# Performance work log

Measured on AMD Instinct MI355X. Metric: run time of the kernel, lower is better.

Reference implementation:

```python
import jax, jax.numpy as jnp
import numpy as np

B, N, D_IN, D_OUT, H = 4, 2048, 1024, 1024, 16
HEAD_DIM = D_OUT // H


def setup_inputs() -> dict:
    key = jax.random.key(0)
    k1, k2, k3 = jax.random.split(key, 3)
    x = jax.random.normal(k1, (B, N, D_IN), dtype=jnp.float32)
    # torch Linear: y = x @ W.T + b; we store W already transposed as [in, out]
    w_attn = jax.random.normal(k2, (D_IN, 3 * D_OUT), dtype=jnp.float32) * (1.0 / np.sqrt(D_IN))
    w_proj = jax.random.normal(k3, (D_OUT, D_OUT), dtype=jnp.float32) * (1.0 / np.sqrt(D_OUT))
    b_proj = jnp.zeros((D_OUT,), dtype=jnp.float32)
    return {"x": x, "w_attn": w_attn, "w_proj": w_proj, "b_proj": b_proj}


def reference(x, w_attn, w_proj, b_proj):
    b, n, _ = x.shape
    qkv = x @ w_attn  # [b, n, 3*d_out]
    q, k, v = jnp.split(qkv, 3, axis=2)
    # [b, n, d_out] -> [b, h, n, head_dim]
    def to_heads(t):
        return t.reshape(b, n, H, HEAD_DIM).transpose(0, 2, 1, 3)
    q, k, v = to_heads(q), to_heads(k), to_heads(v)
    scale = 1.0 / np.sqrt(HEAD_DIM).astype(np.float32)
    att = jnp.einsum('bhqd,bhkd->bhqk', q, k) * scale  # [b, h, n, n]
    causal = jnp.tril(jnp.ones((n, n), dtype=bool))  # True = keep
    att = jnp.where(causal, att, -jnp.inf)
    att = jax.nn.softmax(att, axis=-1)
    # dropout p=0.0 -> identity
    out = jnp.einsum('bhqk,bhkd->bhqd', att, v)  # [b, h, n, head_dim]
    out = out.transpose(0, 2, 1, 3).reshape(b, n, D_OUT)
    return out @ w_proj + b_proj
```

## Files before the change

kernel.cpp:

```cpp
#include <hip/hip_runtime.h>
#include <hip/hip_bf16.h>
#include <stdint.h>

typedef short short8 __attribute__((ext_vector_type(8)));
typedef float f32x4 __attribute__((ext_vector_type(4)));

#define BQ 4
#define NSEQ 2048
#define DMODEL 1024
#define NHEAD 16
#define HDIM 64
#define MTOT 8192
#define QKV_LD 3072

#if __has_builtin(__builtin_amdgcn_exp2f)
#define EXP2(x) __builtin_amdgcn_exp2f(x)
#else
#define EXP2(x) exp2f(x)
#endif
#define C_SCL 0.18033688f
#define THR_RAW 16.635532f

__device__ __forceinline__ uint16_t f2bf(float f) {
  uint32_t u = __builtin_bit_cast(uint32_t, f);
  uint32_t r = (u + 0x7FFFu + ((u >> 16) & 1u)) >> 16;
  return (uint16_t)r;
}
__device__ __forceinline__ uint16_t f2bf_hw(float f) {
  __hip_bfloat16 h = __float2bfloat16(f);
  return __builtin_bit_cast(uint16_t, h);
}

__global__ void cast_f32_bf16_k(const float* __restrict__ in, uint16_t* __restrict__ out, int n) {
  int idx = (blockIdx.x * blockDim.x + threadIdx.x) * 4;
  int stride = gridDim.x * blockDim.x * 4;
  for (int i = idx; i < n; i += stride) {
    float4 v = *reinterpret_cast<const float4*>(in + i);
    ushort4 o;
    o.x = f2bf(v.x); o.y = f2bf(v.y); o.z = f2bf(v.z); o.w = f2bf(v.w);
    *reinterpret_cast<ushort4*>(out + i) = o;
  }
}

__global__ void transpose_cast_k(const float* __restrict__ in, uint16_t* __restrict__ out, int K, int N) {
  __shared__ float tile[32][33];
  int n0 = blockIdx.x * 32;
  int k0 = blockIdx.y * 32;
  int tx = threadIdx.x & 31;
  int ty = threadIdx.x >> 5;
#pragma unroll
  for (int r = 0; r < 4; ++r)
    tile[ty + r * 8][tx] = in[(size_t)(k0 + ty + r * 8) * N + n0 + tx];
  __syncthreads();
#pragma unroll
  for (int r = 0; r < 4; ++r)
    out[(size_t)(n0 + ty + r * 8) * K + k0 + tx] = f2bf(tile[tx][ty + r * 8]);
}

template <bool BF16_OUT>
__global__ void __launch_bounds__(256, 2)
gemm_bt_k(const uint16_t* __restrict__ A, const uint16_t* __restrict__ BT,
          void* __restrict__ Cout, const float* __restrict__ bias,
          int M, int N, int K) {
  __shared__ uint16_t As[128 * 32];
  __shared__ uint16_t Bs[128 * 32];
  const int tid = threadIdx.x;
  const int lane = tid & 63;
  const int wave = tid >> 6;
  const int wr = wave >> 1, wc = wave & 1;
  const int brow = blockIdx.y * 128;
  const int bcol = blockIdx.x * 128;
  const int l16 = lane & 15;
  const int lq = lane >> 4;

  f32x4 acc[4][4];
  const f32x4 fzero = {0.f, 0.f, 0.f, 0.f};
#pragma unroll
  for (int i = 0; i < 4; ++i)
#pragma unroll
    for (int j = 0; j < 4; ++j) acc[i][j] = fzero;

  const int ca = tid, cb = tid + 256;
  const size_t ga0 = (size_t)(brow + (ca >> 2)) * K + (ca & 3) * 8;
  const size_t ga1 = (size_t)(brow + (cb >> 2)) * K + (cb & 3) * 8;
  const size_t gb0 = (size_t)(bcol + (ca >> 2)) * K + (ca & 3) * 8;
  const size_t gb1 = (size_t)(bcol + (cb >> 2)) * K + (cb & 3) * 8;

  for (int kt = 0; kt < K; kt += 32) {
    __builtin_amdgcn_global_load_lds(
        (const __attribute__((address_space(1))) void*)(A + ga0 + kt),
        (__attribute__((address_space(3))) void*)&As[ca * 8], 16, 0, 0);
    __builtin_amdgcn_global_load_lds(
        (const __attribute__((address_space(1))) void*)(A + ga1 + kt),
        (__attribute__((address_space(3))) void*)&As[cb * 8], 16, 0, 0);
    __builtin_amdgcn_global_load_lds(
        (const __attribute__((address_space(1))) void*)(BT + gb0 + kt),
        (__attribute__((address_space(3))) void*)&Bs[ca * 8], 16, 0, 0);
    __builtin_amdgcn_global_load_lds(
        (const __attribute__((address_space(1))) void*)(BT + gb1 + kt),
        (__attribute__((address_space(3))) void*)&Bs[cb * 8], 16, 0, 0);
    __syncthreads();
    short8 af[4], bfr[4];
#pragma unroll
    for (int r = 0; r < 4; ++r) {
      af[r]  = *reinterpret_cast<const short8*>(&As[(wr * 64 + r * 16 + l16) * 32 + lq * 8]);
      bfr[r] = *reinterpret_cast<const short8*>(&Bs[(wc * 64 + r * 16 + l16) * 32 + lq * 8]);
    }
#pragma unroll
    for (int r = 0; r < 4; ++r)
#pragma unroll
      for (int c = 0; c < 4; ++c)
        acc[r][c] = __builtin_amdgcn_mfma_f32_16x16x32_bf16(af[r], bfr[c], acc[r][c], 0, 0, 0);
    __syncthreads();
  }

#pragma unroll
  for (int r = 0; r < 4; ++r) {
    const int row0 = brow + wr * 64 + r * 16 + lq * 4;
#pragma unroll
    for (int c = 0; c < 4; ++c) {
      const int col = bcol + wc * 64 + c * 16 + l16;
#pragma unroll
      for (int i = 0; i < 4; ++i) {
        if constexpr (BF16_OUT)
          reinterpret_cast<uint16_t*>(Cout)[(size_t)(row0 + i) * N + col] = f2bf(acc[r][c][i]);
        else
          reinterpret_cast<float*>(Cout)[(size_t)(row0 + i) * N + col] = acc[r][c][i] + bias[col];
      }
    }
  }
}

__global__ void __launch_bounds__(256, 3)
attn_fwd_k(const uint16_t* __restrict__ qkv, uint16_t* __restrict__ outb) {
  const int obid = blockIdx.x;
  const int bid = (obid & 7) * 128 + (obid >> 3);
  const int p = bid & 15;
  const int h = (bid >> 4) & 15;
  const int b = bid >> 8;
  const int qtA = p;
  const int qtB = 31 - p;
  const int tid = threadIdx.x;
  const int lane = tid & 63;
  const int w = tid >> 6;
  const int l16 = lane & 15;
  const int lq = lane >> 4;

  __shared__ uint16_t Ks[64 * 72];
  __shared__ uint16_t Vt[64 * 72];

  short8 qaA0, qaA1, qaB0, qaB1;
  {
    const size_t baseA = ((size_t)(b * NSEQ + qtA * 64 + w * 16 + l16)) * QKV_LD + h * 64 + lq * 8;
    const size_t baseB = ((size_t)(b * NSEQ + qtB * 64 + w * 16 + l16)) * QKV_LD + h * 64 + lq * 8;
    qaA0 = *reinterpret_cast<const short8*>(qkv + baseA);
    qaA1 = *reinterpret_cast<const short8*>(qkv + baseA + 32);
    qaB0 = *reinterpret_cast<const short8*>(qkv + baseB);
    qaB1 = *reinterpret_cast<const short8*>(qkv + baseB + 32);
  }

  float mA = -1e30f, lA = 0.f, mB = -1e30f, lB = 0.f;
  f32x4 accA[4], accB[4];
  const f32x4 fzero = {0.f, 0.f, 0.f, 0.f};
#pragma unroll
  for (int i = 0; i < 4; ++i) { accA[i] = fzero; accB[i] = fzero; }

  const int r0 = tid >> 3, d0 = (tid & 7) * 8;
  const int ka0 = r0 * 72 + d0;
  const int ka1 = (r0 + 32) * 72 + d0;
  const int lqt = (r0 >> 2) & 3;
  const int nc0 = r0 >> 4;
  const int m0 = d0 >> 3;
  const int jo = (nc0 & 1) * 4 + (r0 & 3);
  const int vcol0 = (((2 * lqt) ^ m0) * 8) + jo;
  const int vcol1 = (((2 * lqt + 1) ^ m0) * 8) + jo;

  const int ntiles = qtB + 1;
  short8 rk0, rk1, rv0, rv1;
  {
    const size_t g0 = ((size_t)(b * NSEQ + r0)) * QKV_LD + 1024 + h * 64 + d0;
    const size_t g1 = ((size_t)(b * NSEQ + r0 + 32)) * QKV_LD + 1024 + h * 64 + d0;
    rk0 = *reinterpret_cast<const short8*>(qkv + g0);
    rv0 = *reinterpret_cast<const short8*>(qkv + g0 + 1024);
    rk1 = *reinterpret_cast<const short8*>(qkv + g1);
    rv1 = *reinterpret_cast<const short8*>(qkv + g1 + 1024);
  }

#define SOFTMAX_PV(SV, M_I, L_I, ACC, DIAG)                                     \
  {                                                                             \
    float tmax_ = -3e38f;                                                       \
    if (DIAG) {                                                                 \
      _Pragma("unroll") for (int nc = 0; nc < 4; ++nc) {                        \
        _Pragma("unroll") for (int i = 0; i < 4; ++i) {                         \
          float v_ = SV[nc][i];                                                 \
          if ((nc * 16 + lq * 4 + i) > (w * 16 + l16)) v_ = -3e38f;             \
          SV[nc][i] = v_;                                                       \
          tmax_ = fmaxf(tmax_, v_);                                             \
        }                                                                       \
      }                                                                         \
    } else {                                                                    \
      _Pragma("unroll") for (int nc = 0; nc < 4; ++nc)                          \
        tmax_ = fmaxf(tmax_, fmaxf(fmaxf(SV[nc][0], SV[nc][1]),                 \
                                   fmaxf(SV[nc][2], SV[nc][3])));               \
    }                                                                           \
    tmax_ = fmaxf(tmax_, __shfl_xor(tmax_, 16, 64));                            \
    tmax_ = fmaxf(tmax_, __shfl_xor(tmax_, 32, 64));                            \
    if (!__all(tmax_ <= M_I + THR_RAW)) {                                       \
      const float mn_ = fmaxf(M_I, tmax_);                                      \
      const float alpha_ = EXP2((M_I - mn_) * C_SCL);                           \
      M_I = mn_;                                                                \
      L_I *= alpha_;                                                            \
      float ab_[4];                                                             \
      _Pragma("unroll") for (int i = 0; i < 4; ++i)                             \
        ab_[i] = __shfl(alpha_, lq * 4 + i, 64);                                \
      _Pragma("unroll") for (int d4 = 0; d4 < 4; ++d4)                          \
        _Pragma("unroll") for (int i = 0; i < 4; ++i)                           \
          ACC[d4][i] *= ab_[i];                                                 \
    }                                                                           \
    const float mc_ = M_I * C_SCL;                                              \
    float rsum_ = 0.f;                                                          \
    short8 pa0_, pa1_;                                                          \
    _Pragma("unroll") for (int nc = 0; nc < 4; ++nc) {                          \
      _Pragma("unroll") for (int i = 0; i < 4; ++i) {                           \
        float pv_ = EXP2(__builtin_fmaf(SV[nc][i], C_SCL, -mc_));               \
        rsum_ += pv_;                                                           \
        uint16_t ph_ = f2bf_hw(pv_);                                            \
        if (nc < 2) pa0_[nc * 4 + i] = (short)ph_;                              \
        else        pa1_[(nc - 2) * 4 + i] = (short)ph_;                        \
      }                                                                         \
    }                                                                           \
    rsum_ += __shfl_xor(rsum_, 16, 64);                                         \
    rsum_ += __shfl_xor(rsum_, 32, 64);                                         \
    L_I += rsum_;                                                               \
    _Pragma("unroll") for (int d4 = 0; d4 < 4; ++d4) {                          \
      const int drow_ = d4 * 16 + l16;                                          \
      const int xr_ = (drow_ >> 3) & 7;                                         \
      short8 vb0_ = *reinterpret_cast<const short8*>(&Vt[drow_ * 72 + (((2 * lq) ^ xr_) * 8)]); \
      short8 vb1_ = *reinterpret_cast<const short8*>(&Vt[drow_ * 72 + (((2 * lq + 1) ^ xr_) * 8)]); \
      ACC[d4] = __builtin_amdgcn_mfma_f32_16x16x32_bf16(pa0_, vb0_, ACC[d4], 0, 0, 0); \
      ACC[d4] = __builtin_amdgcn_mfma_f32_16x16x32_bf16(pa1_, vb1_, ACC[d4], 0, 0, 0); \
    }                                                                           \
  }

  for (int jt = 0; jt < ntiles; ++jt) {
    *reinterpret_cast<short8*>(&Ks[ka0]) = rk0;
    *reinterpret_cast<short8*>(&Ks[ka1]) = rk1;
#pragma unroll
    for (int j = 0; j < 8; ++j) Vt[(d0 + j) * 72 + vcol0] = (uint16_t)rv0[j];
#pragma unroll
    for (int j = 0; j < 8; ++j) Vt[(d0 + j) * 72 + vcol1] = (uint16_t)rv1[j];
    if (jt + 1 < ntiles) {
      const size_t g0 = ((size_t)(b * NSEQ + (jt + 1) * 64 + r0)) * QKV_LD + 1024 + h * 64 + d0;
      const size_t g1 = ((size_t)(b * NSEQ + (jt + 1) * 64 + r0 + 32)) * QKV_LD + 1024 + h * 64 + d0;
      rk0 = *reinterpret_cast<const short8*>(qkv + g0);
      rv0 = *reinterpret_cast<const short8*>(qkv + g0 + 1024);
      rk1 = *reinterpret_cast<const short8*>(qkv + g1);
      rv1 = *reinterpret_cast<const short8*>(qkv + g1 + 1024);
    }
    __syncthreads();

    {
      f32x4 sv[4];
#pragma unroll
      for (int nc = 0; nc < 4; ++nc) {
        short8 kb0 = *reinterpret_cast<const short8*>(&Ks[(nc * 16 + l16) * 72 + lq * 8]);
        short8 kb1 = *reinterpret_cast<const short8*>(&Ks[(nc * 16 + l16) * 72 + 32 + lq * 8]);
        f32x4 s = fzero;
        s = __builtin_amdgcn_mfma_f32_16x16x32_bf16(kb0, qaB0, s, 0, 0, 0);
        s = __builtin_amdgcn_mfma_f32_16x16x32_bf16(kb1, qaB1, s, 0, 0, 0);
        sv[nc] = s;
      }
      SOFTMAX_PV(sv, mB, lB, accB, jt == qtB);
    }

    if (jt <= qtA) {
      f32x4 sv[4];
#pragma unroll
      for (int nc = 0; nc < 4; ++nc) {
        short8 kb0 = *reinterpret_cast<const short8*>(&Ks[(nc * 16 + l16) * 72 + lq * 8]);
        short8 kb1 = *reinterpret_cast<const short8*>(&Ks[(nc * 16 + l16) * 72 + 32 + lq * 8]);
        f32x4 s = fzero;
        s = __builtin_amdgcn_mfma_f32_16x16x32_bf16(kb0, qaA0, s, 0, 0, 0);
        s = __builtin_amdgcn_mfma_f32_16x16x32_bf16(kb1, qaA1, s, 0, 0, 0);
        sv[nc] = s;
      }
      SOFTMAX_PV(sv, mA, lA, accA, jt == qtA);
    }

    __syncthreads();
  }

  {
    float lb4[4];
#pragma unroll
    for (int i = 0; i < 4; ++i) lb4[i] = __shfl(lA, lq * 4 + i, 64);
    const size_t orow = (size_t)(b * NSEQ) + qtA * 64 + w * 16 + lq * 4;
#pragma unroll
    for (int d4 = 0; d4 < 4; ++d4)
#pragma unroll
      for (int i = 0; i < 4; ++i)
        outb[(orow + i) * (size_t)DMODEL + h * 64 + d4 * 16 + l16] = f2bf(accA[d4][i] / lb4[i]);
  }
  {
    float lb4[4];
#pragma unroll
    for (int i = 0; i < 4; ++i) lb4[i] = __shfl(lB, lq * 4 + i, 64);
    const size_t orow = (size_t)(b * NSEQ) + qtB * 64 + w * 16 + lq * 4;
#pragma unroll
    for (int d4 = 0; d4 < 4; ++d4)
#pragma unroll
      for (int i = 0; i < 4; ++i)
        outb[(orow + i) * (size_t)DMODEL + h * 64 + d4 * 16 + l16] = f2bf(accB[d4][i] / lb4[i]);
  }
}

extern "C" void kernel_launch(void* const* d_in, const int* in_sizes, int n_in,
                              void* d_out, int out_size, void* d_ws, size_t ws_size,
                              hipStream_t stream) {
  const float* x      = (const float*)d_in[0];
  const float* w_attn = (const float*)d_in[1];
  const float* w_proj = (const float*)d_in[2];
  const float* b_proj = (const float*)d_in[3];

  uint16_t* xb    = (uint16_t*)d_ws;
  uint16_t* wat   = xb   + (size_t)MTOT * DMODEL;
  uint16_t* wpt   = wat  + (size_t)3072 * 1024;
  uint16_t* qkvb  = wpt  + (size_t)1024 * 1024;
  uint16_t* attnb = qkvb + (size_t)MTOT * QKV_LD;

  cast_f32_bf16_k<<<2048, 256, 0, stream>>>(x, xb, MTOT * DMODEL);
  transpose_cast_k<<<dim3(3072 / 32, 1024 / 32), 256, 0, stream>>>(w_attn, wat, 1024, 3072);
  transpose_cast_k<<<dim3(1024 / 32, 1024 / 32), 256, 0, stream>>>(w_proj, wpt, 1024, 1024);

  gemm_bt_k<true><<<dim3(3072 / 128, MTOT / 128), 256, 0, stream>>>(
      xb, wat, qkvb, nullptr, MTOT, 3072, 1024);

  attn_fwd_k<<<BQ * NHEAD * 16, 256, 0, stream>>>(qkvb, attnb);

  gemm_bt_k<false><<<dim3(1024 / 128, MTOT / 128), 256, 0, stream>>>(
      attnb, wpt, d_out, b_proj, MTOT, 1024, 1024);
}
```

Measured before the change: 188.3 us.

## Split causal attention KV range across two blocks and merge partial softmax results

The attention kernel launches twice as many blocks. Each block handles one of two KV-tile ranges for its paired query tiles, with split points chosen so both halves do roughly equal work. Each half writes an unnormalized bf16 partial output plus its per-row running max and sum, and a new merge kernel rescales and combines the two partials into the final normalized attention output. The goal is more parallelism and a smaller wave-quantization tail on the GPU. The cost is an extra kernel launch, extra memory traffic for the partials (one buffer reuses the x bf16 workspace), and some precision loss from storing unnormalized partials in bf16.

```diff
diff --git a/kernel.cpp b/kernel.cpp
--- a/kernel.cpp
+++ b/kernel.cpp
@@ -29,6 +29,10 @@
 __device__ __forceinline__ uint16_t f2bf_hw(float f) {
   __hip_bfloat16 h = __float2bfloat16(f);
   return __builtin_bit_cast(uint16_t, h);
+}
+__device__ __forceinline__ float bf2f(uint16_t h) {
+  uint32_t u = ((uint32_t)h) << 16;
+  return __builtin_bit_cast(float, u);
 }
 
 __global__ void cast_f32_bf16_k(const float* __restrict__ in, uint16_t* __restrict__ out, int n) {
@@ -132,12 +136,14 @@
 }
 
 __global__ void __launch_bounds__(256, 3)
-attn_fwd_k(const uint16_t* __restrict__ qkv, uint16_t* __restrict__ outb) {
+attn_fwd_k(const uint16_t* __restrict__ qkv, uint16_t* __restrict__ ph0,
+           uint16_t* __restrict__ ph1, float* __restrict__ pml) {
   const int obid = blockIdx.x;
-  const int bid = (obid & 7) * 128 + (obid >> 3);
+  const int bid = (obid & 7) * 256 + (obid >> 3);
   const int p = bid & 15;
   const int h = (bid >> 4) & 15;
-  const int b = bid >> 8;
+  const int half = (bid >> 8) & 1;
+  const int b = bid >> 9;
   const int qtA = p;
   const int qtB = 31 - p;
   const int tid = threadIdx.x;
@@ -148,6 +154,11 @@
 
   __shared__ uint16_t Ks[64 * 72];
   __shared__ uint16_t Vt[64 * 72];
+
+  const int ntiles = qtB + 1;
+  const int mid = (p >= 7) ? 8 : (16 - p);
+  const int lo = half ? mid : 0;
+  const int hi = half ? ntiles : mid;
 
   short8 qaA0, qaA1, qaB0, qaB1;
   {
@@ -175,11 +186,10 @@
   const int vcol0 = (((2 * lqt) ^ m0) * 8) + jo;
   const int vcol1 = (((2 * lqt + 1) ^ m0) * 8) + jo;
 
-  const int ntiles = qtB + 1;
   short8 rk0, rk1, rv0, rv1;
   {
-    const size_t g0 = ((size_t)(b * NSEQ + r0)) * QKV_LD + 1024 + h * 64 + d0;
-    const size_t g1 = ((size_t)(b * NSEQ + r0 + 32)) * QKV_LD + 1024 + h * 64 + d0;
+    const size_t g0 = ((size_t)(b * NSEQ + lo * 64 + r0)) * QKV_LD + 1024 + h * 64 + d0;
+    const size_t g1 = ((size_t)(b * NSEQ + lo * 64 + r0 + 32)) * QKV_LD + 1024 + h * 64 + d0;
     rk0 = *reinterpret_cast<const short8*>(qkv + g0);
     rv0 = *reinterpret_cast<const short8*>(qkv + g0 + 1024);
     rk1 = *reinterpret_cast<const short8*>(qkv + g1);
@@ -242,14 +252,14 @@
     }                                                                           \
   }
 
-  for (int jt = 0; jt < ntiles; ++jt) {
+  for (int jt = lo; jt < hi; ++jt) {
     *reinterpret_cast<short8*>(&Ks[ka0]) = rk0;
     *reinterpret_cast<short8*>(&Ks[ka1]) = rk1;
 #pragma unroll
     for (int j = 0; j < 8; ++j) Vt[(d0 + j) * 72 + vcol0] = (uint16_t)rv0[j];
 #pragma unroll
     for (int j = 0; j < 8; ++j) Vt[(d0 + j) * 72 + vcol1] = (uint16_t)rv1[j];
-    if (jt + 1 < ntiles) {
+    if (jt + 1 < hi) {
       const size_t g0 = ((size_t)(b * NSEQ + (jt + 1) * 64 + r0)) * QKV_LD + 1024 + h * 64 + d0;
       const size_t g1 = ((size_t)(b * NSEQ + (jt + 1) * 64 + r0 + 32)) * QKV_LD + 1024 + h * 64 + d0;
       rk0 = *reinterpret_cast<const short8*>(qkv + g0);
@@ -290,28 +300,52 @@
     __syncthreads();
   }
 
+  uint16_t* ph = half ? ph1 : ph0;
   {
-    float lb4[4];
-#pragma unroll
-    for (int i = 0; i < 4; ++i) lb4[i] = __shfl(lA, lq * 4 + i, 64);
     const size_t orow = (size_t)(b * NSEQ) + qtA * 64 + w * 16 + lq * 4;
 #pragma unroll
     for (int d4 = 0; d4 < 4; ++d4)
 #pragma unroll
       for (int i = 0; i < 4; ++i)
-        outb[(orow + i) * (size_t)DMODEL + h * 64 + d4 * 16 + l16] = f2bf(accA[d4][i] / lb4[i]);
+        ph[(orow + i) * (size_t)DMODEL + h * 64 + d4 * 16 + l16] = f2bf_hw(accA[d4][i]);
   }
   {
-    float lb4[4];
-#pragma unroll
-    for (int i = 0; i < 4; ++i) lb4[i] = __shfl(lB, lq * 4 + i, 64);
     const size_t orow = (size_t)(b * NSEQ) + qtB * 64 + w * 16 + lq * 4;
 #pragma unroll
     for (int d4 = 0; d4 < 4; ++d4)
 #pragma unroll
       for (int i = 0; i < 4; ++i)
-        outb[(orow + i) * (size_t)DMODEL + h * 64 + d4 * 16 + l16] = f2bf(accB[d4][i] / lb4[i]);
-  }
+        ph[(orow + i) * (size_t)DMODEL + h * 64 + d4 * 16 + l16] = f2bf_hw(accB[d4][i]);
+  }
+  if (lq == 0) {
+    const size_t rowA = (size_t)(b * NSEQ) + qtA * 64 + w * 16 + l16;
+    const size_t rowB = (size_t)(b * NSEQ) + qtB * 64 + w * 16 + l16;
+    const size_t iA = (rowA * NHEAD + h) * 4 + half * 2;
+    const size_t iB = (rowB * NHEAD + h) * 4 + half * 2;
+    pml[iA] = mA; pml[iA + 1] = lA;
+    pml[iB] = mB; pml[iB + 1] = lB;
+  }
+}
+
+__global__ void attn_merge_k(const uint16_t* __restrict__ ph0, const uint16_t* __restrict__ ph1,
+                             const float* __restrict__ pml, uint16_t* __restrict__ outb) {
+  const size_t base = ((size_t)blockIdx.x * 256 + threadIdx.x) * 8;
+  const int row = (int)(base >> 10);
+  const int h = (int)((base & 1023) >> 6);
+  const float4 q = *reinterpret_cast<const float4*>(pml + ((size_t)row * NHEAD + h) * 4);
+  const float ms = fmaxf(q.x, q.z);
+  const float a0 = EXP2((q.x - ms) * C_SCL);
+  const float a1 = EXP2((q.z - ms) * C_SCL);
+  const float inv = 1.f / (q.y * a0 + q.w * a1);
+  short8 v0 = *reinterpret_cast<const short8*>(ph0 + base);
+  short8 v1 = *reinterpret_cast<const short8*>(ph1 + base);
+  short8 o;
+#pragma unroll
+  for (int j = 0; j < 8; ++j) {
+    float f = (bf2f((uint16_t)v0[j]) * a0 + bf2f((uint16_t)v1[j]) * a1) * inv;
+    o[j] = (short)f2bf_hw(f);
+  }
+  *reinterpret_cast<short8*>(outb + base) = o;
 }
 
 extern "C" void kernel_launch(void* const* d_in, const int* in_sizes, int n_in,
@@ -327,6 +361,9 @@
   uint16_t* wpt   = wat  + (size_t)3072 * 1024;
   uint16_t* qkvb  = wpt  + (size_t)1024 * 1024;
   uint16_t* attnb = qkvb + (size_t)MTOT * QKV_LD;
+  uint16_t* ph1   = attnb + (size_t)MTOT * DMODEL;
+  float*    pml   = (float*)(ph1 + (size_t)MTOT * DMODEL);
+  uint16_t* ph0   = xb;
 
   cast_f32_bf16_k<<<2048, 256, 0, stream>>>(x, xb, MTOT * DMODEL);
   transpose_cast_k<<<dim3(3072 / 32, 1024 / 32), 256, 0, stream>>>(w_attn, wat, 1024, 3072);
@@ -335,7 +372,8 @@
   gemm_bt_k<true><<<dim3(3072 / 128, MTOT / 128), 256, 0, stream>>>(
       xb, wat, qkvb, nullptr, MTOT, 3072, 1024);
 
-  attn_fwd_k<<<BQ * NHEAD * 16, 256, 0, stream>>>(qkvb, attnb);
+  attn_fwd_k<<<BQ * NHEAD * 16 * 2, 256, 0, stream>>>(qkvb, ph0, ph1, pml);
+  attn_merge_k<<<(MTOT * DMODEL) / (8 * 256), 256, 0, stream>>>(ph0, ph1, pml, attnb);
 
   gemm_bt_k<false><<<dim3(1024 / 128, MTOT / 128), 256, 0, stream>>>(
       attnb, wpt, d_out, b_proj, MTOT, 1024, 1024);
```

After: 199.3 us. 1.06x slower.
